# Kernel optimization log

Hardware: AMD Instinct MI355X
Metric: run time of the kernel (lower is better)

The kernel has to match this reference:

```python
import jax, jax.numpy as jnp
import numpy as np

N, E, IN_FEATS, D, H, DIST_DIM, NBOUND = 10000, 160000, 128, 64, 4, 32, 31

def setup_inputs() -> dict:
    key = jax.random.key(0)
    ks = jax.random.split(key, 16)
    gain = 5.0 / 3.0  # tanh gain
    def xavier(k, shape):
        # xavier_normal over the last two dims (fan_in, fan_out) as torch does per-slice
        fan_in, fan_out = shape[-2], shape[-1]
        std = gain * np.sqrt(2.0 / (fan_in + fan_out))
        return jax.random.normal(k, shape, dtype=jnp.float32) * std
    inp = {
        'feat': jax.random.normal(ks[0], (N, IN_FEATS), dtype=jnp.float32),
        'locations': jax.random.normal(ks[1], (N, 3), dtype=jnp.float32),
        'src': jax.random.randint(ks[2], (E,), 0, N),
        'dst': jax.random.randint(ks[3], (E,), 0, N),
        'inter_ids': jax.random.randint(ks[4], (E, H), 0, N),
        'W_fc': xavier(ks[5], (IN_FEATS, H * D)),
        'embed_table': jax.random.normal(ks[6], (NBOUND + 1, DIST_DIM), dtype=jnp.float32),
        'G': xavier(ks[7], (H, DIST_DIM, D)),
        'attn_fc1': xavier(ks[8], (H, 2 * D, D)),
        'attn_fc2': xavier(ks[9], (H, 2 * D, D)),
        'attn_fc3': xavier(ks[10], (H, 2 * D, D)),
        'attn_fc': xavier(ks[11], (H, 3 * D, D)),
        'attn_out': xavier(ks[12], (H, D, 1)),
        'boundaries': jnp.linspace(0.1, 3.1, NBOUND).astype(jnp.float32),
    }
    return inp


def reference(feat, locations, W_fc, embed_table, G, attn_fc1, attn_fc2, attn_fc3,
              attn_fc, attn_out, boundaries, src, dst, inter_ids):
    n = feat.shape[0]
    h = (feat @ W_fc).reshape(n, H, D)                      # [N,H,D]
    pos = locations                                          # [N,3]
    src_pos = pos[src]                                       # [E,3]
    dst_pos = pos[dst]                                       # [E,3]
    inter_pos = pos[inter_ids]                               # [E,H,3]
    h_src = h[src]                                           # [E,H,D]
    h_dst = h[dst]                                           # [E,H,D]
    head_idx = jnp.arange(H)[None, :]
    inter_h = h[inter_ids, head_idx, :]                      # [E,H,D] per-head gather

    e_count = src.shape[0]
    dist1 = jnp.broadcast_to(jnp.linalg.norm(dst_pos - src_pos, axis=-1)[:, None], (e_count, H))
    dist2 = jnp.linalg.norm(dst_pos[:, None, :] - inter_pos, axis=-1)   # [E,H]
    dist_ = jnp.linalg.norm(src_pos[:, None, :] - inter_pos, axis=-1)   # [E,H]

    def dist_embed(dist):
        idx = jnp.searchsorted(boundaries, dist, side='left')  # torch.bucketize(right=False)
        e = embed_table[idx]                                   # [E,H,DIST_DIM]
        return jnp.einsum('ehk,hkd->ehd', e, G)                # [E,H,D]

    de1 = dist_embed(dist1)
    de2 = dist_embed(dist2)
    de_ = dist_embed(dist_)

    d1 = jnp.einsum('ehk,hkd->ehd', jnp.concatenate([h_src, de1], axis=-1), attn_fc1)
    d2 = jnp.einsum('ehk,hkd->ehd', jnp.concatenate([inter_h, de2], axis=-1), attn_fc2)
    d3 = jnp.einsum('ehk,hkd->ehd', jnp.concatenate([h_dst, de_], axis=-1), attn_fc3)

    h_c = jnp.tanh(jnp.einsum('ehk,hkd->ehd', jnp.concatenate([d1, d2, d3], axis=-1), attn_fc))
    e_score = jnp.einsum('ehd,hdo->eho', h_c, attn_out)[..., 0]        # [E,H]

    # edge softmax grouped by destination node
    m = jax.ops.segment_max(e_score, dst, num_segments=n)              # [N,H]
    ex = jnp.exp(e_score - m[dst])
    den = jax.ops.segment_sum(ex, dst, num_segments=n)                 # [N,H]
    a = ex / den[dst]                                                  # [E,H]

    ft = jax.ops.segment_sum(a[:, :, None] * h_src, dst, num_segments=n)  # [N,H,D]
    rst = jnp.mean(ft, axis=1)                                          # merge='mean' -> [N,D]
    return rst
```

## Files before the change

### kernel.cpp

```cpp
#include <hip/hip_runtime.h>
#include <hip/hip_fp16.h>
#include <math.h>

#define N_NODES 10000
#define E_EDGES 160000
#define DMODEL 64
#define H 4
#define NBOUND 31
#define SLOTS 64
#define QREC 1024

typedef _Float16 half8 __attribute__((ext_vector_type(8)));
typedef float floatx4 __attribute__((ext_vector_type(4)));

__device__ __forceinline__ void mm4(const float* __restrict__ S, int aoff,
                                    int astride, int boff, int i0, int j,
                                    int Kdim, float o[4]) {
  float a0 = 0.f, a1 = 0.f, a2 = 0.f, a3 = 0.f;
  for (int t4 = 0; t4 < (Kdim >> 2); ++t4) {
    float4 f0 = *(const float4*)&S[aoff + (i0 + 0) * astride + t4 * 4];
    float4 f1 = *(const float4*)&S[aoff + (i0 + 1) * astride + t4 * 4];
    float4 f2 = *(const float4*)&S[aoff + (i0 + 2) * astride + t4 * 4];
    float4 f3 = *(const float4*)&S[aoff + (i0 + 3) * astride + t4 * 4];
    float b0 = S[boff + (t4 * 4 + 0) * 64 + j];
    float b1 = S[boff + (t4 * 4 + 1) * 64 + j];
    float b2 = S[boff + (t4 * 4 + 2) * 64 + j];
    float b3 = S[boff + (t4 * 4 + 3) * 64 + j];
    a0 += f0.x * b0 + f0.y * b1 + f0.z * b2 + f0.w * b3;
    a1 += f1.x * b0 + f1.y * b1 + f1.z * b2 + f1.w * b3;
    a2 += f2.x * b0 + f2.y * b1 + f2.z * b2 + f2.w * b3;
    a3 += f3.x * b0 + f3.y * b1 + f3.z * b2 + f3.w * b3;
  }
  o[0] = a0; o[1] = a1; o[2] = a2; o[3] = a3;
}

__device__ __forceinline__ int didx(const float* __restrict__ bnd2, float d) {
  int g = (int)(d * 10.0f);
  g = (g < 0) ? 0 : ((g > 31) ? 31 : g);
  g += (bnd2[g + 1] < d) ? 1 : 0;
  g -= (bnd2[g] >= d) ? 1 : 0;
  return g;
}

__global__ __launch_bounds__(256) void edge_kernel(
    const float* __restrict__ pos, const int* __restrict__ src,
    const int* __restrict__ dst, const int* __restrict__ inter,
    const float* __restrict__ boundaries, int* __restrict__ cnt,
    uint4* __restrict__ ebuf) {
  __shared__ float Sb[48];
  int tid = threadIdx.x;
  if (tid < NBOUND) Sb[tid + 1] = boundaries[tid];
  if (tid == NBOUND) { Sb[0] = -INFINITY; Sb[32] = INFINITY; }
  __syncthreads();
  int e = blockIdx.x * 256 + tid;
  int s = src[e], t = dst[e];
  int4 iv = *(const int4*)&inter[e * 4];
  int itarr[4] = {iv.x, iv.y, iv.z, iv.w};
  float sx = pos[s * 3], sy = pos[s * 3 + 1], sz = pos[s * 3 + 2];
  float tx = pos[t * 3], ty = pos[t * 3 + 1], tz = pos[t * 3 + 2];
  float dx = tx - sx, dy = ty - sy, dz = tz - sz;
  float dist1 = sqrtf(dx * dx + dy * dy + dz * dz);
  unsigned i1 = (unsigned)didx(Sb, dist1);
  unsigned w3 = 0, q20 = 0, q_0 = 0;
  #pragma unroll
  for (int hh = 0; hh < 4; ++hh) {
    int it = itarr[hh];
    float ix = pos[it * 3], iy = pos[it * 3 + 1], iz = pos[it * 3 + 2];
    float ax = tx - ix, ay = ty - iy, az = tz - iz;
    float dist2 = sqrtf(ax * ax + ay * ay + az * az);
    float bx = sx - ix, by = sy - iy, bz = sz - iz;
    float dist_ = sqrtf(bx * bx + by * by + bz * bz);
    unsigned idx2 = (unsigned)didx(Sb, dist2);
    unsigned idx_ = (unsigned)didx(Sb, dist_);
    if (hh == 0) { q20 = idx2; q_0 = idx_; }
    else w3 |= (idx2 | (idx_ << 5)) << ((hh - 1) * 10);
  }
  uint4 rec;
  rec.x = (unsigned)s | ((unsigned)itarr[0] << 16);
  rec.y = (unsigned)itarr[1] | ((unsigned)itarr[2] << 16);
  rec.z = (unsigned)itarr[3] | (i1 << 16) | (q20 << 21) | (q_0 << 26);
  rec.w = w3;
  int p = atomicAdd(&cnt[t], 1);
  if (p < SLOTS) ebuf[t * SLOTS + p] = rec;
}

__global__ __launch_bounds__(512) void prep_kernel(
    const float* __restrict__ fc1, const float* __restrict__ fc2,
    const float* __restrict__ fc3, const float* __restrict__ fcc,
    const float* __restrict__ Wfc, const float* __restrict__ G,
    const float* __restrict__ emb, __half* __restrict__ bigWT,
    __half* __restrict__ U16) {
  __shared__ __align__(16) float S[12288];
  int bi = blockIdx.x;
  int tid = threadIdx.x;
  int chain = (bi >= 12);
  int kh = chain ? (bi - 12) : bi;
  int k = kh >> 2, h = kh & 3;
  const float* fck = (k == 0) ? fc1 : (k == 1) ? fc2 : fc3;
  fck += h * 128 * 64;
  const float* F = fcc + h * 192 * 64 + k * 64 * 64;
  int j = tid & 63, ig = tid >> 6;
  float o[4];
  if (!chain) {
    #pragma unroll
    for (int u = 0; u < 2; ++u) {
      ((float4*)S)[u * 512 + tid] = ((const float4*)F)[u * 512 + tid];
      ((float4*)(S + 4096))[u * 512 + tid] = ((const float4*)fck)[u * 512 + tid];
    }
    __syncthreads();
    #pragma unroll
    for (int rg = 0; rg < 2; ++rg) {
      int i0 = ig * 8 + rg * 4;
      mm4(S, 4096, 64, 0, i0, j, 64, o);
      S[8192 + (i0 + 0) * 64 + j] = o[0];
      S[8192 + (i0 + 1) * 64 + j] = o[1];
      S[8192 + (i0 + 2) * 64 + j] = o[2];
      S[8192 + (i0 + 3) * 64 + j] = o[3];
    }
    __syncthreads();
    #pragma unroll
    for (int u = 0; u < 2; ++u) {
      int fi = u * 512 + tid;
      int i = fi >> 4, c4 = fi & 15;
      ((float4*)(S + 4096))[fi] = ((const float4*)(Wfc + i * 256 + h * 64))[c4];
    }
    __syncthreads();
    if (k == 0) {
      #pragma unroll
      for (int u = 0; u < 8; ++u) {
        int idx = u * 512 + tid;
        int i = idx >> 6, jj = idx & 63;
        bigWT[(h * 64 + jj) * 128 + i] = __float2half(S[4096 + idx]);
      }
    }
    #pragma unroll
    for (int rg = 0; rg < 2; ++rg) {
      int i0 = ig * 8 + rg * 4;
      mm4(S, 4096, 64, 8192, i0, j, 64, o);
      int rb = ((k + 1) * 256 + h * 64 + j) * 128;
      bigWT[rb + i0 + 0] = __float2half(o[0]);
      bigWT[rb + i0 + 1] = __float2half(o[1]);
      bigWT[rb + i0 + 2] = __float2half(o[2]);
      bigWT[rb + i0 + 3] = __float2half(o[3]);
    }
    __syncthreads();
    #pragma unroll
    for (int u = 0; u < 2; ++u) {
      int fi = u * 512 + tid;
      int i = fi >> 4, c4 = fi & 15;
      ((float4*)(S + 4096))[fi] =
          ((const float4*)(Wfc + (64 + i) * 256 + h * 64))[c4];
    }
    __syncthreads();
    if (k == 0) {
      #pragma unroll
      for (int u = 0; u < 8; ++u) {
        int idx = u * 512 + tid;
        int i = idx >> 6, jj = idx & 63;
        bigWT[(h * 64 + jj) * 128 + 64 + i] = __float2half(S[4096 + idx]);
      }
    }
    #pragma unroll
    for (int rg = 0; rg < 2; ++rg) {
      int i0 = ig * 8 + rg * 4;
      mm4(S, 4096, 64, 8192, i0, j, 64, o);
      int rb = ((k + 1) * 256 + h * 64 + j) * 128;
      bigWT[rb + 64 + i0 + 0] = __float2half(o[0]);
      bigWT[rb + 64 + i0 + 1] = __float2half(o[1]);
      bigWT[rb + 64 + i0 + 2] = __float2half(o[2]);
      bigWT[rb + 64 + i0 + 3] = __float2half(o[3]);
    }
    return;
  }
  #pragma unroll
  for (int u = 0; u < 2; ++u) {
    ((float4*)S)[u * 512 + tid] = ((const float4*)F)[u * 512 + tid];
    ((float4*)(S + 4096))[u * 512 + tid] =
        ((const float4*)(fck + 4096))[u * 512 + tid];
  }
  __syncthreads();
  #pragma unroll
  for (int rg = 0; rg < 2; ++rg) {
    int i0 = ig * 8 + rg * 4;
    mm4(S, 4096, 64, 0, i0, j, 64, o);
    S[8192 + (i0 + 0) * 64 + j] = o[0];
    S[8192 + (i0 + 1) * 64 + j] = o[1];
    S[8192 + (i0 + 2) * 64 + j] = o[2];
    S[8192 + (i0 + 3) * 64 + j] = o[3];
  }
  __syncthreads();
  ((float4*)S)[tid] = ((const float4*)(G + h * 2048))[tid];
  if (tid < 256) ((float4*)(S + 2048))[tid] = ((const float4*)emb)[tid];
  __syncthreads();
  {
    int i0 = ig * 4;
    mm4(S, 0, 64, 8192, i0, j, 64, o);
    S[3072 + (i0 + 0) * 64 + j] = o[0];
    S[3072 + (i0 + 1) * 64 + j] = o[1];
    S[3072 + (i0 + 2) * 64 + j] = o[2];
    S[3072 + (i0 + 3) * 64 + j] = o[3];
  }
  __syncthreads();
  {
    int i0 = ig * 4;
    mm4(S, 2048, 32, 3072, i0, j, 32, o);
    int base = k * 8192 + h * 2048;
    U16[base + (i0 + 0) * 64 + j] = __float2half(o[0]);
    U16[base + (i0 + 1) * 64 + j] = __float2half(o[1]);
    U16[base + (i0 + 2) * 64 + j] = __float2half(o[2]);
    U16[base + (i0 + 3) * 64 + j] = __float2half(o[3]);
  }
}

#define EROW 264

__global__ __launch_bounds__(256) void gemm_kernel(
    const float* __restrict__ feat, const __half* __restrict__ bigWT,
    __half* __restrict__ qall) {
  __shared__ __align__(16) __half Esm[4][16][EROW];
  int bi = blockIdx.x;
  int tid = threadIdx.x;
  int bx = bi % 157, by = bi / 157;
  int wv = tid >> 6, l = tid & 63;
  int m0 = bx * 64 + wv * 16;
  int n0 = by * 256;
  int lm = l & 15, lk = (l >> 4) * 8;
  int arow = m0 + lm;
  if (arow >= N_NODES) arow = N_NODES - 1;
  const float* fp = feat + arow * 128 + lk;
  const _Float16* bp = (const _Float16*)bigWT + lk;
  half8 a[4];
  #pragma unroll
  for (int kt = 0; kt < 4; ++kt) {
    float4 u0 = *(const float4*)(fp + kt * 32);
    float4 u1 = *(const float4*)(fp + kt * 32 + 4);
    half8 t;
    t[0] = (_Float16)u0.x; t[1] = (_Float16)u0.y;
    t[2] = (_Float16)u0.z; t[3] = (_Float16)u0.w;
    t[4] = (_Float16)u1.x; t[5] = (_Float16)u1.y;
    t[6] = (_Float16)u1.z; t[7] = (_Float16)u1.w;
    a[kt] = t;
  }
  #pragma unroll
  for (int nt = 0; nt < 16; ++nt) {
    floatx4 acc = (floatx4){0.f, 0.f, 0.f, 0.f};
    #pragma unroll
    for (int kt = 0; kt < 4; ++kt) {
      half8 b = *(const half8*)(bp + (n0 + nt * 16 + lm) * 128 + kt * 32);
      acc = __builtin_amdgcn_mfma_f32_16x16x32_f16(a[kt], b, acc, 0, 0, 0);
    }
    int dd = nt * 16 + lm;
    int o = (by == 0) ? ((dd & 63) * 4 + (dd >> 6)) : dd;
    #pragma unroll
    for (int r4 = 0; r4 < 4; ++r4)
      Esm[wv][(l >> 4) * 4 + r4][o] = __float2half(acc[r4]);
  }
  __syncthreads();
  int row = l >> 2;
  int j0 = (l & 3) * 64;
  int m = m0 + row;
  if (m < N_NODES) {
    #pragma unroll
    for (int u = 0; u < 8; ++u) {
      uint4 v = *(const uint4*)&Esm[wv][row][j0 + u * 8];
      *(uint4*)&qall[m * QREC + by * 256 + j0 + u * 8] = v;
    }
  }
}

__device__ __forceinline__ float dpp_row_sum16(float v) {
  int x;
  x = __builtin_amdgcn_update_dpp(0, __float_as_int(v), 0x128, 0xf, 0xf, true);
  v += __int_as_float(x);
  x = __builtin_amdgcn_update_dpp(0, __float_as_int(v), 0x124, 0xf, 0xf, true);
  v += __int_as_float(x);
  x = __builtin_amdgcn_update_dpp(0, __float_as_int(v), 0x122, 0xf, 0xf, true);
  v += __int_as_float(x);
  x = __builtin_amdgcn_update_dpp(0, __float_as_int(v), 0x121, 0xf, 0xf, true);
  v += __int_as_float(x);
  return v;
}

union H4u { uint2 u; __half2 h[2]; };

__device__ __forceinline__ float tanh_dot(H4u A, H4u B, H4u C, H4u X, H4u Y,
                                          H4u Z, float4 a4) {
  __half2 z0 = __hadd2(__hadd2(A.h[0], B.h[0]), __hadd2(C.h[0], X.h[0]));
  z0 = __hadd2(z0, __hadd2(Y.h[0], Z.h[0]));
  __half2 z1 = __hadd2(__hadd2(A.h[1], B.h[1]), __hadd2(C.h[1], X.h[1]));
  z1 = __hadd2(z1, __hadd2(Y.h[1], Z.h[1]));
  float2 f0 = __half22float2(z0);
  float2 f1 = __half22float2(z1);
  const float K = 2.885390082f;
  float p0 = __builtin_amdgcn_exp2f(f0.x * K);
  float p1 = __builtin_amdgcn_exp2f(f0.y * K);
  float p2 = __builtin_amdgcn_exp2f(f1.x * K);
  float p3 = __builtin_amdgcn_exp2f(f1.y * K);
  float r0 = __builtin_amdgcn_rcpf(p0 + 1.0f);
  float r1 = __builtin_amdgcn_rcpf(p1 + 1.0f);
  float r2 = __builtin_amdgcn_rcpf(p2 + 1.0f);
  float r3 = __builtin_amdgcn_rcpf(p3 + 1.0f);
  float dot = a4.x * r0;
  dot = fmaf(a4.y, r1, dot);
  dot = fmaf(a4.z, r2, dot);
  dot = fmaf(a4.w, r3, dot);
  float asum = (a4.x + a4.y) + (a4.z + a4.w);
  return fmaf(-2.0f, dot, asum);
}

__device__ __forceinline__ float4 h4_to_f4(uint2 u) {
  union { uint2 ui; __half2 h[2]; } cc;
  cc.ui = u;
  float2 a = __half22float2(cc.h[0]);
  float2 b = __half22float2(cc.h[1]);
  return make_float4(a.x, a.y, b.x, b.y);
}

__device__ __forceinline__ void dec_rec(uint4 r, int h, int* s, int* it,
                                        unsigned* i1, unsigned* q2,
                                        unsigned* q_) {
  *s = (int)(r.x & 0xffff);
  *it = (h == 0) ? (int)(r.x >> 16)
      : (h == 1) ? (int)(r.y & 0xffff)
      : (h == 2) ? (int)(r.y >> 16) : (int)(r.z & 0xffff);
  *i1 = (r.z >> 16) & 31;
  if (h == 0) {
    *q2 = (r.z >> 21) & 31;
    *q_ = (r.z >> 26) & 31;
  } else {
    unsigned f = r.w >> ((h - 1) * 10);
    *q2 = f & 31;
    *q_ = (f >> 5) & 31;
  }
}

__device__ __forceinline__ void gather_edge(
    const __half* __restrict__ qall, const __half* __restrict__ U16, int h,
    int c, int lane, int s, int it, unsigned i1, unsigned q2, unsigned q_,
    H4u* A, H4u* B, H4u* X, H4u* Y, H4u* Z, uint2* hr) {
  A->u = *(const uint2*)(qall + s * QREC + 256 + h * 64 + c * 4);
  B->u = *(const uint2*)(qall + it * QREC + 512 + h * 64 + c * 4);
  X->u = *(const uint2*)(U16 + (h * 32 + (int)i1) * 64 + c * 4);
  Y->u = *(const uint2*)(U16 + 8192 + (h * 32 + (int)q2) * 64 + c * 4);
  Z->u = *(const uint2*)(U16 + 16384 + (h * 32 + (int)q_) * 64 + c * 4);
  *hr = *(const uint2*)(qall + s * QREC + lane * 4);
}

__global__ __launch_bounds__(256) void score_agg_kernel(
    const int* __restrict__ cnt, const uint4* __restrict__ ebuf,
    const __half* __restrict__ qall, const __half* __restrict__ U16,
    const float* __restrict__ aout, float* __restrict__ out) {
  __shared__ uint4 recs[4][SLOTS];
  int tid = threadIdx.x;
  int w = tid >> 6, lane = tid & 63;
  int h = lane >> 4, c = lane & 15;
  int n = blockIdx.x * 4 + w;
  int deg = cnt[n];
  if (deg > SLOTS) deg = SLOTS;
  if (lane < deg) recs[w][lane] = ebuf[n * SLOTS + lane];
  H4u C;
  C.u = *(const uint2*)(qall + n * QREC + 768 + h * 64 + c * 4);
  const float4 a4 = *((const float4*)(aout + h * 64) + c);
  __syncthreads();
  float4 num = make_float4(0.f, 0.f, 0.f, 0.f);
  float4 den = make_float4(0.f, 0.f, 0.f, 0.f);
  for (int i = 0; i < deg; i += 2) {
    int iB = i + 1;
    int vB = (iB < deg);
    uint4 rA = recs[w][i];
    uint4 rB = recs[w][vB ? iB : i];
    int sA, itA, sB, itB;
    unsigned i1A, q2A, q_A, i1B, q2B, q_B;
    dec_rec(rA, h, &sA, &itA, &i1A, &q2A, &q_A);
    dec_rec(rB, h, &sB, &itB, &i1B, &q2B, &q_B);
    H4u A0, B0, X0, Y0, Z0, A1, B1, X1, Y1, Z1;
    uint2 hr0, hr1;
    gather_edge(qall, U16, h, c, lane, sA, itA, i1A, q2A, q_A, &A0, &B0, &X0,
                &Y0, &Z0, &hr0);
    gather_edge(qall, U16, h, c, lane, sB, itB, i1B, q2B, q_B, &A1, &B1, &X1,
                &Y1, &Z1, &hr1);
    float v0 = tanh_dot(A0, B0, C, X0, Y0, Z0, a4);
    float v1 = tanh_dot(A1, B1, C, X1, Y1, Z1, a4);
    v0 = dpp_row_sum16(v0);
    v1 = dpp_row_sum16(v1);
    float ex0 = __expf(v0);
    float ex1 = vB ? __expf(v1) : 0.f;
    float4 hv0 = h4_to_f4(hr0);
    float4 hv1 = h4_to_f4(hr1);
    float e00 = __shfl(ex0, 0), e01 = __shfl(ex0, 16);
    float e02 = __shfl(ex0, 32), e03 = __shfl(ex0, 48);
    float e10 = __shfl(ex1, 0), e11 = __shfl(ex1, 16);
    float e12 = __shfl(ex1, 32), e13 = __shfl(ex1, 48);
    num.x += e00 * hv0.x + e10 * hv1.x;
    num.y += e01 * hv0.y + e11 * hv1.y;
    num.z += e02 * hv0.z + e12 * hv1.z;
    num.w += e03 * hv0.w + e13 * hv1.w;
    den.x += e00 + e10;
    den.y += e01 + e11;
    den.z += e02 + e12;
    den.w += e03 + e13;
  }
  float r = 0.f;
  if (deg > 0)
    r = 0.25f * (num.x / den.x + num.y / den.y + num.z / den.z + num.w / den.w);
  out[n * 64 + lane] = r;
}

extern "C" void kernel_launch(void* const* d_in, const int* in_sizes, int n_in,
                              void* d_out, int out_size, void* d_ws,
                              size_t ws_size, hipStream_t stream) {
  const float* feat = (const float*)d_in[0];
  const float* loc = (const float*)d_in[1];
  const int* src = (const int*)d_in[2];
  const int* dst = (const int*)d_in[3];
  const int* inter = (const int*)d_in[4];
  const float* Wfc = (const float*)d_in[5];
  const float* emb = (const float*)d_in[6];
  const float* G = (const float*)d_in[7];
  const float* fc1 = (const float*)d_in[8];
  const float* fc2 = (const float*)d_in[9];
  const float* fc3 = (const float*)d_in[10];
  const float* fcc = (const float*)d_in[11];
  const float* aout = (const float*)d_in[12];
  const float* bnd = (const float*)d_in[13];
  float* out = (float*)d_out;

  __half* qall = (__half*)d_ws;
  __half* bigWT = qall + N_NODES * QREC;
  __half* U16 = bigWT + 1024 * 128;
  uint4* ebuf = (uint4*)(U16 + 3 * H * 2048);
  int* cnt = (int*)(ebuf + N_NODES * SLOTS);

  hipMemsetAsync(cnt, 0, N_NODES * sizeof(int), stream);
  edge_kernel<<<E_EDGES / 256, 256, 0, stream>>>(loc, src, dst, inter, bnd,
                                                 cnt, ebuf);
  prep_kernel<<<24, 512, 0, stream>>>(fc1, fc2, fc3, fcc, Wfc, G, emb, bigWT,
                                      U16);
  gemm_kernel<<<628, 256, 0, stream>>>(feat, bigWT, qall);
  score_agg_kernel<<<N_NODES / 4, 256, 0, stream>>>(cnt, ebuf, qall, U16, aout,
                                                    out);
}
```

Measured before the change: 191.3 us.

## Fuse edge binning into GEMM launch, zero counters in prep, one node per block

Removes the memset and the separate edge kernel by zeroing the counters in extra prep_kernel blocks and running the edge bucketing as extra blocks of the GEMM launch. This cuts the launch count from five to three. The score/aggregate kernel now gives each node a whole 256-thread block, with four waves splitting its edges four at a time, and combines the partial sums through shared memory. That adds parallelism and memory-level concurrency per node, but costs a block-wide reduction and leaves many waves idle on low-degree nodes.

```diff
diff --git a/kernel.cpp b/kernel.cpp
--- a/kernel.cpp
+++ b/kernel.cpp
@@ -42,57 +42,20 @@
   return g;
 }
 
-__global__ __launch_bounds__(256) void edge_kernel(
-    const float* __restrict__ pos, const int* __restrict__ src,
-    const int* __restrict__ dst, const int* __restrict__ inter,
-    const float* __restrict__ boundaries, int* __restrict__ cnt,
-    uint4* __restrict__ ebuf) {
-  __shared__ float Sb[48];
-  int tid = threadIdx.x;
-  if (tid < NBOUND) Sb[tid + 1] = boundaries[tid];
-  if (tid == NBOUND) { Sb[0] = -INFINITY; Sb[32] = INFINITY; }
-  __syncthreads();
-  int e = blockIdx.x * 256 + tid;
-  int s = src[e], t = dst[e];
-  int4 iv = *(const int4*)&inter[e * 4];
-  int itarr[4] = {iv.x, iv.y, iv.z, iv.w};
-  float sx = pos[s * 3], sy = pos[s * 3 + 1], sz = pos[s * 3 + 2];
-  float tx = pos[t * 3], ty = pos[t * 3 + 1], tz = pos[t * 3 + 2];
-  float dx = tx - sx, dy = ty - sy, dz = tz - sz;
-  float dist1 = sqrtf(dx * dx + dy * dy + dz * dz);
-  unsigned i1 = (unsigned)didx(Sb, dist1);
-  unsigned w3 = 0, q20 = 0, q_0 = 0;
-  #pragma unroll
-  for (int hh = 0; hh < 4; ++hh) {
-    int it = itarr[hh];
-    float ix = pos[it * 3], iy = pos[it * 3 + 1], iz = pos[it * 3 + 2];
-    float ax = tx - ix, ay = ty - iy, az = tz - iz;
-    float dist2 = sqrtf(ax * ax + ay * ay + az * az);
-    float bx = sx - ix, by = sy - iy, bz = sz - iz;
-    float dist_ = sqrtf(bx * bx + by * by + bz * bz);
-    unsigned idx2 = (unsigned)didx(Sb, dist2);
-    unsigned idx_ = (unsigned)didx(Sb, dist_);
-    if (hh == 0) { q20 = idx2; q_0 = idx_; }
-    else w3 |= (idx2 | (idx_ << 5)) << ((hh - 1) * 10);
-  }
-  uint4 rec;
-  rec.x = (unsigned)s | ((unsigned)itarr[0] << 16);
-  rec.y = (unsigned)itarr[1] | ((unsigned)itarr[2] << 16);
-  rec.z = (unsigned)itarr[3] | (i1 << 16) | (q20 << 21) | (q_0 << 26);
-  rec.w = w3;
-  int p = atomicAdd(&cnt[t], 1);
-  if (p < SLOTS) ebuf[t * SLOTS + p] = rec;
-}
-
 __global__ __launch_bounds__(512) void prep_kernel(
     const float* __restrict__ fc1, const float* __restrict__ fc2,
     const float* __restrict__ fc3, const float* __restrict__ fcc,
     const float* __restrict__ Wfc, const float* __restrict__ G,
     const float* __restrict__ emb, __half* __restrict__ bigWT,
-    __half* __restrict__ U16) {
+    __half* __restrict__ U16, int* __restrict__ cnt) {
   __shared__ __align__(16) float S[12288];
   int bi = blockIdx.x;
   int tid = threadIdx.x;
+  if (bi >= 24) {
+    int n = (bi - 24) * 512 + tid;
+    if (n < N_NODES) cnt[n] = 0;
+    return;
+  }
   int chain = (bi >= 12);
   int kh = chain ? (bi - 12) : bi;
   int k = kh >> 2, h = kh & 3;
@@ -214,12 +177,52 @@
 
 #define EROW 264
 
-__global__ __launch_bounds__(256) void gemm_kernel(
+__global__ __launch_bounds__(256) void gemm_edge_kernel(
     const float* __restrict__ feat, const __half* __restrict__ bigWT,
-    __half* __restrict__ qall) {
+    __half* __restrict__ qall, const float* __restrict__ pos,
+    const int* __restrict__ src, const int* __restrict__ dst,
+    const int* __restrict__ inter, const float* __restrict__ boundaries,
+    int* __restrict__ cnt, uint4* __restrict__ ebuf) {
   __shared__ __align__(16) __half Esm[4][16][EROW];
+  __shared__ float Sb[48];
   int bi = blockIdx.x;
   int tid = threadIdx.x;
+  if (bi >= 628) {
+    if (tid < NBOUND) Sb[tid + 1] = boundaries[tid];
+    if (tid == NBOUND) { Sb[0] = -INFINITY; Sb[32] = INFINITY; }
+    __syncthreads();
+    int e = (bi - 628) * 256 + tid;
+    int s = src[e], t = dst[e];
+    int4 iv = *(const int4*)&inter[e * 4];
+    int itarr[4] = {iv.x, iv.y, iv.z, iv.w};
+    float sx = pos[s * 3], sy = pos[s * 3 + 1], sz = pos[s * 3 + 2];
+    float tx = pos[t * 3], ty = pos[t * 3 + 1], tz = pos[t * 3 + 2];
+    float dx = tx - sx, dy = ty - sy, dz = tz - sz;
+    float dist1 = sqrtf(dx * dx + dy * dy + dz * dz);
+    unsigned i1 = (unsigned)didx(Sb, dist1);
+    unsigned w3 = 0, q20 = 0, q_0 = 0;
+    #pragma unroll
+    for (int hh = 0; hh < 4; ++hh) {
+      int it = itarr[hh];
+      float ix = pos[it * 3], iy = pos[it * 3 + 1], iz = pos[it * 3 + 2];
+      float ax = tx - ix, ay = ty - iy, az = tz - iz;
+      float dist2 = sqrtf(ax * ax + ay * ay + az * az);
+      float bx = sx - ix, by = sy - iy, bz = sz - iz;
+      float dist_ = sqrtf(bx * bx + by * by + bz * bz);
+      unsigned idx2 = (unsigned)didx(Sb, dist2);
+      unsigned idx_ = (unsigned)didx(Sb, dist_);
+      if (hh == 0) { q20 = idx2; q_0 = idx_; }
+      else w3 |= (idx2 | (idx_ << 5)) << ((hh - 1) * 10);
+    }
+    uint4 rec;
+    rec.x = (unsigned)s | ((unsigned)itarr[0] << 16);
+    rec.y = (unsigned)itarr[1] | ((unsigned)itarr[2] << 16);
+    rec.z = (unsigned)itarr[3] | (i1 << 16) | (q20 << 21) | (q_0 << 26);
+    rec.w = w3;
+    int p = atomicAdd(&cnt[t], 1);
+    if (p < SLOTS) ebuf[t * SLOTS + p] = rec;
+    return;
+  }
   int bx = bi % 157, by = bi / 157;
   int wv = tid >> 6, l = tid & 63;
   int m0 = bx * 64 + wv * 16;
@@ -350,60 +353,77 @@
     const int* __restrict__ cnt, const uint4* __restrict__ ebuf,
     const __half* __restrict__ qall, const __half* __restrict__ U16,
     const float* __restrict__ aout, float* __restrict__ out) {
-  __shared__ uint4 recs[4][SLOTS];
+  __shared__ uint4 recs[SLOTS];
+  __shared__ float4 sm_num[4][64];
+  __shared__ float4 sm_den[4];
   int tid = threadIdx.x;
   int w = tid >> 6, lane = tid & 63;
   int h = lane >> 4, c = lane & 15;
-  int n = blockIdx.x * 4 + w;
+  int n = blockIdx.x;
   int deg = cnt[n];
   if (deg > SLOTS) deg = SLOTS;
-  if (lane < deg) recs[w][lane] = ebuf[n * SLOTS + lane];
+  if (tid < deg) recs[tid] = ebuf[n * SLOTS + tid];
   H4u C;
   C.u = *(const uint2*)(qall + n * QREC + 768 + h * 64 + c * 4);
   const float4 a4 = *((const float4*)(aout + h * 64) + c);
   __syncthreads();
   float4 num = make_float4(0.f, 0.f, 0.f, 0.f);
   float4 den = make_float4(0.f, 0.f, 0.f, 0.f);
-  for (int i = 0; i < deg; i += 2) {
-    int iB = i + 1;
-    int vB = (iB < deg);
-    uint4 rA = recs[w][i];
-    uint4 rB = recs[w][vB ? iB : i];
-    int sA, itA, sB, itB;
-    unsigned i1A, q2A, q_A, i1B, q2B, q_B;
-    dec_rec(rA, h, &sA, &itA, &i1A, &q2A, &q_A);
-    dec_rec(rB, h, &sB, &itB, &i1B, &q2B, &q_B);
-    H4u A0, B0, X0, Y0, Z0, A1, B1, X1, Y1, Z1;
-    uint2 hr0, hr1;
-    gather_edge(qall, U16, h, c, lane, sA, itA, i1A, q2A, q_A, &A0, &B0, &X0,
-                &Y0, &Z0, &hr0);
-    gather_edge(qall, U16, h, c, lane, sB, itB, i1B, q2B, q_B, &A1, &B1, &X1,
-                &Y1, &Z1, &hr1);
-    float v0 = tanh_dot(A0, B0, C, X0, Y0, Z0, a4);
-    float v1 = tanh_dot(A1, B1, C, X1, Y1, Z1, a4);
-    v0 = dpp_row_sum16(v0);
-    v1 = dpp_row_sum16(v1);
-    float ex0 = __expf(v0);
-    float ex1 = vB ? __expf(v1) : 0.f;
-    float4 hv0 = h4_to_f4(hr0);
-    float4 hv1 = h4_to_f4(hr1);
-    float e00 = __shfl(ex0, 0), e01 = __shfl(ex0, 16);
-    float e02 = __shfl(ex0, 32), e03 = __shfl(ex0, 48);
-    float e10 = __shfl(ex1, 0), e11 = __shfl(ex1, 16);
-    float e12 = __shfl(ex1, 32), e13 = __shfl(ex1, 48);
-    num.x += e00 * hv0.x + e10 * hv1.x;
-    num.y += e01 * hv0.y + e11 * hv1.y;
-    num.z += e02 * hv0.z + e12 * hv1.z;
-    num.w += e03 * hv0.w + e13 * hv1.w;
-    den.x += e00 + e10;
-    den.y += e01 + e11;
-    den.z += e02 + e12;
-    den.w += e03 + e13;
-  }
-  float r = 0.f;
-  if (deg > 0)
-    r = 0.25f * (num.x / den.x + num.y / den.y + num.z / den.z + num.w / den.w);
-  out[n * 64 + lane] = r;
+  for (int i = w; i < deg; i += 16) {
+    int val[4];
+    uint4 r[4];
+    #pragma unroll
+    for (int u = 0; u < 4; ++u) {
+      int idx = i + 4 * u;
+      val[u] = (idx < deg);
+      r[u] = recs[val[u] ? idx : i];
+    }
+    int s[4], it[4];
+    unsigned i1[4], q2[4], q_[4];
+    #pragma unroll
+    for (int u = 0; u < 4; ++u)
+      dec_rec(r[u], h, &s[u], &it[u], &i1[u], &q2[u], &q_[u]);
+    H4u A[4], B[4], X[4], Y[4], Z[4];
+    uint2 hr[4];
+    #pragma unroll
+    for (int u = 0; u < 4; ++u)
+      gather_edge(qall, U16, h, c, lane, s[u], it[u], i1[u], q2[u], q_[u],
+                  &A[u], &B[u], &X[u], &Y[u], &Z[u], &hr[u]);
+    float v[4];
+    #pragma unroll
+    for (int u = 0; u < 4; ++u)
+      v[u] = tanh_dot(A[u], B[u], C, X[u], Y[u], Z[u], a4);
+    #pragma unroll
+    for (int u = 0; u < 4; ++u) v[u] = dpp_row_sum16(v[u]);
+    #pragma unroll
+    for (int u = 0; u < 4; ++u) {
+      float ex = val[u] ? __expf(v[u]) : 0.f;
+      float e0 = __shfl(ex, 0), e1 = __shfl(ex, 16);
+      float e2 = __shfl(ex, 32), e3 = __shfl(ex, 48);
+      float4 hv = h4_to_f4(hr[u]);
+      num.x += e0 * hv.x;
+      num.y += e1 * hv.y;
+      num.z += e2 * hv.z;
+      num.w += e3 * hv.w;
+      den.x += e0; den.y += e1; den.z += e2; den.w += e3;
+    }
+  }
+  sm_num[w][lane] = num;
+  if (lane == 0) sm_den[w] = den;
+  __syncthreads();
+  if (tid < 64) {
+    float4 n0 = sm_num[0][tid], n1 = sm_num[1][tid];
+    float4 n2 = sm_num[2][tid], n3 = sm_num[3][tid];
+    float4 d0 = sm_den[0], d1 = sm_den[1], d2 = sm_den[2], d3 = sm_den[3];
+    float4 ns = make_float4(n0.x + n1.x + n2.x + n3.x, n0.y + n1.y + n2.y + n3.y,
+                            n0.z + n1.z + n2.z + n3.z, n0.w + n1.w + n2.w + n3.w);
+    float4 ds = make_float4(d0.x + d1.x + d2.x + d3.x, d0.y + d1.y + d2.y + d3.y,
+                            d0.z + d1.z + d2.z + d3.z, d0.w + d1.w + d2.w + d3.w);
+    float r = 0.f;
+    if (deg > 0)
+      r = 0.25f * (ns.x / ds.x + ns.y / ds.y + ns.z / ds.z + ns.w / ds.w);
+    out[n * 64 + tid] = r;
+  }
 }
 
 extern "C" void kernel_launch(void* const* d_in, const int* in_sizes, int n_in,
@@ -431,12 +451,10 @@
   uint4* ebuf = (uint4*)(U16 + 3 * H * 2048);
   int* cnt = (int*)(ebuf + N_NODES * SLOTS);
 
-  hipMemsetAsync(cnt, 0, N_NODES * sizeof(int), stream);
-  edge_kernel<<<E_EDGES / 256, 256, 0, stream>>>(loc, src, dst, inter, bnd,
-                                                 cnt, ebuf);
-  prep_kernel<<<24, 512, 0, stream>>>(fc1, fc2, fc3, fcc, Wfc, G, emb, bigWT,
-                                      U16);
-  gemm_kernel<<<628, 256, 0, stream>>>(feat, bigWT, qall);
-  score_agg_kernel<<<N_NODES / 4, 256, 0, stream>>>(cnt, ebuf, qall, U16, aout,
-                                                    out);
-}
+  prep_kernel<<<44, 512, 0, stream>>>(fc1, fc2, fc3, fcc, Wfc, G, emb, bigWT,
+                                      U16, cnt);
+  gemm_edge_kernel<<<1253, 256, 0, stream>>>(feat, bigWT, qall, loc, src, dst,
+                                             inter, bnd, cnt, ebuf);
+  score_agg_kernel<<<N_NODES, 256, 0, stream>>>(cnt, ebuf, qall, U16, aout,
+                                                out);
+}
```

New measurement: 184.4 us. 1.04x faster.

## Fuse edge bucketing into GEMM launch, zero counts in prep, split node across warps

Applied to the files above, without the earlier changes.

The separate memset and edge bucketing kernel are removed. The count zeroing becomes extra blocks of the prep kernel, and the edge bucketing becomes extra blocks of the GEMM kernel, cutting the launch count from five to three. The aggregation kernel now gives each node a full 256-thread block, with its four warps splitting the node's edges and combining partial sums through shared memory. This is meant to cut launch overhead and balance degree-dependent work across warps, at the cost of an extra block barrier and 4x more blocks in the aggregation pass.

```diff
diff --git a/kernel.cpp b/kernel.cpp
--- a/kernel.cpp
+++ b/kernel.cpp
@@ -42,57 +42,20 @@
   return g;
 }
 
-__global__ __launch_bounds__(256) void edge_kernel(
-    const float* __restrict__ pos, const int* __restrict__ src,
-    const int* __restrict__ dst, const int* __restrict__ inter,
-    const float* __restrict__ boundaries, int* __restrict__ cnt,
-    uint4* __restrict__ ebuf) {
-  __shared__ float Sb[48];
-  int tid = threadIdx.x;
-  if (tid < NBOUND) Sb[tid + 1] = boundaries[tid];
-  if (tid == NBOUND) { Sb[0] = -INFINITY; Sb[32] = INFINITY; }
-  __syncthreads();
-  int e = blockIdx.x * 256 + tid;
-  int s = src[e], t = dst[e];
-  int4 iv = *(const int4*)&inter[e * 4];
-  int itarr[4] = {iv.x, iv.y, iv.z, iv.w};
-  float sx = pos[s * 3], sy = pos[s * 3 + 1], sz = pos[s * 3 + 2];
-  float tx = pos[t * 3], ty = pos[t * 3 + 1], tz = pos[t * 3 + 2];
-  float dx = tx - sx, dy = ty - sy, dz = tz - sz;
-  float dist1 = sqrtf(dx * dx + dy * dy + dz * dz);
-  unsigned i1 = (unsigned)didx(Sb, dist1);
-  unsigned w3 = 0, q20 = 0, q_0 = 0;
-  #pragma unroll
-  for (int hh = 0; hh < 4; ++hh) {
-    int it = itarr[hh];
-    float ix = pos[it * 3], iy = pos[it * 3 + 1], iz = pos[it * 3 + 2];
-    float ax = tx - ix, ay = ty - iy, az = tz - iz;
-    float dist2 = sqrtf(ax * ax + ay * ay + az * az);
-    float bx = sx - ix, by = sy - iy, bz = sz - iz;
-    float dist_ = sqrtf(bx * bx + by * by + bz * bz);
-    unsigned idx2 = (unsigned)didx(Sb, dist2);
-    unsigned idx_ = (unsigned)didx(Sb, dist_);
-    if (hh == 0) { q20 = idx2; q_0 = idx_; }
-    else w3 |= (idx2 | (idx_ << 5)) << ((hh - 1) * 10);
-  }
-  uint4 rec;
-  rec.x = (unsigned)s | ((unsigned)itarr[0] << 16);
-  rec.y = (unsigned)itarr[1] | ((unsigned)itarr[2] << 16);
-  rec.z = (unsigned)itarr[3] | (i1 << 16) | (q20 << 21) | (q_0 << 26);
-  rec.w = w3;
-  int p = atomicAdd(&cnt[t], 1);
-  if (p < SLOTS) ebuf[t * SLOTS + p] = rec;
-}
-
 __global__ __launch_bounds__(512) void prep_kernel(
     const float* __restrict__ fc1, const float* __restrict__ fc2,
     const float* __restrict__ fc3, const float* __restrict__ fcc,
     const float* __restrict__ Wfc, const float* __restrict__ G,
     const float* __restrict__ emb, __half* __restrict__ bigWT,
-    __half* __restrict__ U16) {
+    __half* __restrict__ U16, int* __restrict__ cnt) {
   __shared__ __align__(16) float S[12288];
   int bi = blockIdx.x;
   int tid = threadIdx.x;
+  if (bi >= 24) {
+    int n = (bi - 24) * 512 + tid;
+    if (n < N_NODES) cnt[n] = 0;
+    return;
+  }
   int chain = (bi >= 12);
   int kh = chain ? (bi - 12) : bi;
   int k = kh >> 2, h = kh & 3;
@@ -214,12 +177,52 @@
 
 #define EROW 264
 
-__global__ __launch_bounds__(256) void gemm_kernel(
+__global__ __launch_bounds__(256) void gemm_edge_kernel(
     const float* __restrict__ feat, const __half* __restrict__ bigWT,
-    __half* __restrict__ qall) {
+    __half* __restrict__ qall, const float* __restrict__ pos,
+    const int* __restrict__ src, const int* __restrict__ dst,
+    const int* __restrict__ inter, const float* __restrict__ boundaries,
+    int* __restrict__ cnt, uint4* __restrict__ ebuf) {
   __shared__ __align__(16) __half Esm[4][16][EROW];
+  __shared__ float Sb[48];
   int bi = blockIdx.x;
   int tid = threadIdx.x;
+  if (bi >= 628) {
+    if (tid < NBOUND) Sb[tid + 1] = boundaries[tid];
+    if (tid == NBOUND) { Sb[0] = -INFINITY; Sb[32] = INFINITY; }
+    __syncthreads();
+    int e = (bi - 628) * 256 + tid;
+    int s = src[e], t = dst[e];
+    int4 iv = *(const int4*)&inter[e * 4];
+    int itarr[4] = {iv.x, iv.y, iv.z, iv.w};
+    float sx = pos[s * 3], sy = pos[s * 3 + 1], sz = pos[s * 3 + 2];
+    float tx = pos[t * 3], ty = pos[t * 3 + 1], tz = pos[t * 3 + 2];
+    float dx = tx - sx, dy = ty - sy, dz = tz - sz;
+    float dist1 = sqrtf(dx * dx + dy * dy + dz * dz);
+    unsigned i1 = (unsigned)didx(Sb, dist1);
+    unsigned w3 = 0, q20 = 0, q_0 = 0;
+    #pragma unroll
+    for (int hh = 0; hh < 4; ++hh) {
+      int it = itarr[hh];
+      float ix = pos[it * 3], iy = pos[it * 3 + 1], iz = pos[it * 3 + 2];
+      float ax = tx - ix, ay = ty - iy, az = tz - iz;
+      float dist2 = sqrtf(ax * ax + ay * ay + az * az);
+      float bx = sx - ix, by = sy - iy, bz = sz - iz;
+      float dist_ = sqrtf(bx * bx + by * by + bz * bz);
+      unsigned idx2 = (unsigned)didx(Sb, dist2);
+      unsigned idx_ = (unsigned)didx(Sb, dist_);
+      if (hh == 0) { q20 = idx2; q_0 = idx_; }
+      else w3 |= (idx2 | (idx_ << 5)) << ((hh - 1) * 10);
+    }
+    uint4 rec;
+    rec.x = (unsigned)s | ((unsigned)itarr[0] << 16);
+    rec.y = (unsigned)itarr[1] | ((unsigned)itarr[2] << 16);
+    rec.z = (unsigned)itarr[3] | (i1 << 16) | (q20 << 21) | (q_0 << 26);
+    rec.w = w3;
+    int p = atomicAdd(&cnt[t], 1);
+    if (p < SLOTS) ebuf[t * SLOTS + p] = rec;
+    return;
+  }
   int bx = bi % 157, by = bi / 157;
   int wv = tid >> 6, l = tid & 63;
   int m0 = bx * 64 + wv * 16;
@@ -350,25 +353,27 @@
     const int* __restrict__ cnt, const uint4* __restrict__ ebuf,
     const __half* __restrict__ qall, const __half* __restrict__ U16,
     const float* __restrict__ aout, float* __restrict__ out) {
-  __shared__ uint4 recs[4][SLOTS];
+  __shared__ uint4 recs[SLOTS];
+  __shared__ float4 sm_num[4][64];
+  __shared__ float4 sm_den[4];
   int tid = threadIdx.x;
   int w = tid >> 6, lane = tid & 63;
   int h = lane >> 4, c = lane & 15;
-  int n = blockIdx.x * 4 + w;
+  int n = blockIdx.x;
   int deg = cnt[n];
   if (deg > SLOTS) deg = SLOTS;
-  if (lane < deg) recs[w][lane] = ebuf[n * SLOTS + lane];
+  if (tid < deg) recs[tid] = ebuf[n * SLOTS + tid];
   H4u C;
   C.u = *(const uint2*)(qall + n * QREC + 768 + h * 64 + c * 4);
   const float4 a4 = *((const float4*)(aout + h * 64) + c);
   __syncthreads();
   float4 num = make_float4(0.f, 0.f, 0.f, 0.f);
   float4 den = make_float4(0.f, 0.f, 0.f, 0.f);
-  for (int i = 0; i < deg; i += 2) {
-    int iB = i + 1;
+  for (int i = w; i < deg; i += 8) {
+    int iB = i + 4;
     int vB = (iB < deg);
-    uint4 rA = recs[w][i];
-    uint4 rB = recs[w][vB ? iB : i];
+    uint4 rA = recs[i];
+    uint4 rB = recs[vB ? iB : i];
     int sA, itA, sB, itB;
     unsigned i1A, q2A, q_A, i1B, q2B, q_B;
     dec_rec(rA, h, &sA, &itA, &i1A, &q2A, &q_A);
@@ -400,10 +405,22 @@
     den.z += e02 + e12;
     den.w += e03 + e13;
   }
-  float r = 0.f;
-  if (deg > 0)
-    r = 0.25f * (num.x / den.x + num.y / den.y + num.z / den.z + num.w / den.w);
-  out[n * 64 + lane] = r;
+  sm_num[w][lane] = num;
+  if (lane == 0) sm_den[w] = den;
+  __syncthreads();
+  if (tid < 64) {
+    float4 n0 = sm_num[0][tid], n1 = sm_num[1][tid];
+    float4 n2 = sm_num[2][tid], n3 = sm_num[3][tid];
+    float4 d0 = sm_den[0], d1 = sm_den[1], d2 = sm_den[2], d3 = sm_den[3];
+    float4 ns = make_float4(n0.x + n1.x + n2.x + n3.x, n0.y + n1.y + n2.y + n3.y,
+                            n0.z + n1.z + n2.z + n3.z, n0.w + n1.w + n2.w + n3.w);
+    float4 ds = make_float4(d0.x + d1.x + d2.x + d3.x, d0.y + d1.y + d2.y + d3.y,
+                            d0.z + d1.z + d2.z + d3.z, d0.w + d1.w + d2.w + d3.w);
+    float r = 0.f;
+    if (deg > 0)
+      r = 0.25f * (ns.x / ds.x + ns.y / ds.y + ns.z / ds.z + ns.w / ds.w);
+    out[n * 64 + tid] = r;
+  }
 }
 
 extern "C" void kernel_launch(void* const* d_in, const int* in_sizes, int n_in,
@@ -431,12 +448,10 @@
   uint4* ebuf = (uint4*)(U16 + 3 * H * 2048);
   int* cnt = (int*)(ebuf + N_NODES * SLOTS);
 
-  hipMemsetAsync(cnt, 0, N_NODES * sizeof(int), stream);
-  edge_kernel<<<E_EDGES / 256, 256, 0, stream>>>(loc, src, dst, inter, bnd,
-                                                 cnt, ebuf);
-  prep_kernel<<<24, 512, 0, stream>>>(fc1, fc2, fc3, fcc, Wfc, G, emb, bigWT,
-                                      U16);
-  gemm_kernel<<<628, 256, 0, stream>>>(feat, bigWT, qall);
-  score_agg_kernel<<<N_NODES / 4, 256, 0, stream>>>(cnt, ebuf, qall, U16, aout,
-                                                    out);
-}
+  prep_kernel<<<44, 512, 0, stream>>>(fc1, fc2, fc3, fcc, Wfc, G, emb, bigWT,
+                                      U16, cnt);
+  gemm_edge_kernel<<<1253, 256, 0, stream>>>(feat, bigWT, qall, loc, src, dst,
+                                             inter, bnd, cnt, ebuf);
+  score_agg_kernel<<<N_NODES, 256, 0, stream>>>(cnt, ebuf, qall, U16, aout,
+                                                out);
+}
```

Result: faster. 174.4 us (-8.8%).
